# Optimization experiments

Hardware: AMD Instinct MI355X
Metric: run time of the kernel (lower is better)

## Reference

```python
import jax, jax.numpy as jnp
import numpy as np

B, CIN, COUT, L, K = 4, 512, 512, 4096, 7
DIL, STR = 1, 1
OUT_LEN = (L - DIL * (K - 1) - 1) // STR + 1  # 4090 ('valid' conv output length)


def setup_inputs() -> dict:
    key = jax.random.key(0)
    k1, k2, k3, k4 = jax.random.split(key, 4)
    x = jax.random.normal(k1, (B, CIN, L), dtype=jnp.float32)
    offsets = jax.random.normal(k2, (B, 1, OUT_LEN, K), dtype=jnp.float32)
    # kaiming_uniform_(a=sqrt(5)) on [COUT, CIN, K] -> U(-1/sqrt(fan_in), 1/sqrt(fan_in))
    fan_in = CIN * K
    bound = 1.0 / np.sqrt(fan_in)
    weight = jax.random.uniform(k3, (COUT, CIN, K), dtype=jnp.float32, minval=-bound, maxval=bound)
    bias = jax.random.uniform(k4, (COUT,), dtype=jnp.float32, minval=-bound, maxval=bound)
    return {"x": x, "offsets": offsets, "weight": weight, "bias": bias}


def _deform_interp(x, offsets, kernel_size, dilation, stride):
    # x: [B, C, L]; offsets: [B, 1, out_len, K] (offset_groups == 1)
    Lx = x.shape[-1]
    dil_pos = (jnp.arange(kernel_size) * dilation).astype(offsets.dtype)       # [K]
    out_len = offsets.shape[-2]
    t0s = (jnp.arange(out_len) * stride).astype(offsets.dtype)[:, None]        # [out_len, 1]
    T = t0s + dil_pos + offsets                                                # [B, 1, out_len, K]
    # constrained: each sample must stay inside its receptive field
    T = jnp.maximum(T, t0s)
    T = jnp.minimum(T, t0s + dil_pos[-1])
    U0 = jnp.clip(jnp.floor(T).astype(jnp.int32), 0, Lx - 2)                   # [B, 1, out_len, K]
    U = jnp.stack([U0, U0 + 1], axis=-1)                                       # [B, 1, out_len, K, 2]
    idx = U[:, 0]                                                              # [B, out_len, K, 2]
    # gather along length, broadcast index over channels
    xg = jax.vmap(lambda xb, ib: xb[:, ib])(x, idx)                            # [B, C, out_len, K, 2]
    # linear-interp weights: max(0, 1 - |U - T|)
    G = jnp.maximum(0.0, 1.0 - jnp.abs(U.astype(T.dtype) - T[..., None]))      # [B, 1, out_len, K, 2]
    return jnp.sum(G * xg, axis=-1)                                            # [B, C, out_len, K]


def reference(x, offsets, weight, bias):
    samp = _deform_interp(x, offsets, K, DIL, STR)                             # [B, C, out_len, K]
    # conv1d(weight, stride=K) on flattened [B, C, out_len*K] == per-position full contraction
    out = jnp.einsum('bcok,dck->bdo', samp, weight) + bias[:, None]            # [B, COUT, out_len]
    return out
```

## Files before the change

kernel.cpp:

```cpp
#include <hip/hip_runtime.h>
#include <hip/hip_bf16.h>
#include <stdint.h>

#define B_      4
#define CIN     512
#define COUT    512
#define L_      4096
#define K_      7
#define OUT_LEN 4090

typedef unsigned short ushort_t;
typedef __attribute__((ext_vector_type(8))) __bf16 bf16x8;
typedef __attribute__((ext_vector_type(4))) float f32x4;

__device__ __forceinline__ uint32_t f2bf(float f) {
    uint32_t u = __float_as_uint(f);
    return (u + 0x7fffu + ((u >> 16) & 1u)) >> 16;
}

__device__ __forceinline__ uint32_t pack2bf(float s0, float s1) {
    __hip_bfloat162 h = __float22bfloat162_rn(make_float2(s0, s1));
    uint32_t r;
    __builtin_memcpy(&r, &h, 4);
    return r;
}

__device__ __forceinline__ uint32_t interp1(uint32_t wl, uint32_t wh, float g0, float g1) {
    const float l0 = __uint_as_float(wl << 16);
    const float l1 = __uint_as_float(wl & 0xffff0000u);
    const float h0 = __uint_as_float(wh << 16);
    const float h1 = __uint_as_float(wh & 0xffff0000u);
    return pack2bf(g0 * l0 + g1 * h0, g0 * l1 + g1 * h1);
}

__device__ __forceinline__ void async16(const void* g, void* l) {
    __builtin_amdgcn_global_load_lds(
        (const __attribute__((address_space(1))) unsigned int*)g,
        (__attribute__((address_space(3))) unsigned int*)l, 16, 0, 0);
}


__global__ __launch_bounds__(256)
void reorder_w2_kernel(const float* __restrict__ w, uint32_t* __restrict__ Wr) {
    const int d   = blockIdx.x;
    const int tid = threadIdx.x;
    __shared__ float wrow[3584];
    const float4* src = (const float4*)(w + (size_t)d * 3584);
    for (int e = tid; e < 896; e += 256) ((float4*)wrow)[e] = src[e];
    __syncthreads();
    const int cc  = tid >> 4;
    const int clp = tid & 15;
    const int pos = (((clp >> 2) ^ ((d >> 1) & 3)) << 2) | (clp & 3);
    #pragma unroll
    for (int k = 0; k < K_; ++k) {
        const float w0 = wrow[tid * 14 + k];
        const float w1 = wrow[tid * 14 + 7 + k];
        Wr[((size_t)(cc * 7 + k) * 512 + d) * 16 + pos] = (f2bf(w1) << 16) | f2bf(w0);
    }
}

__global__ __launch_bounds__(256)
void interp_pack_kernel(const float* __restrict__ x, const float* __restrict__ offs,
                        uint32_t* __restrict__ P) {
    const int obx = blockIdx.x;
    const int cc  = blockIdx.y;
    const int b   = blockIdx.z;
    const int tid = threadIdx.x;
    const int o0  = obx * 128;
    __shared__ __align__(16) uint32_t XT[2176];

    const float* xc = x + ((size_t)b * CIN + cc * 32) * L_ + o0;
    #pragma unroll
    for (int r = 0; r < 3; ++r) {
        const int e = r * 256 + tid;
        if (e < 544) {
            const int cp   = e / 34;
            const int col4 = e - cp * 34;
            const int colb = col4 * 4;
            const float* p0 = xc + (size_t)(2 * cp) * L_ + colb;
            const float* p1 = p0 + L_;
            float4 v0, v1;
            if (o0 + colb + 3 < L_) {
                v0 = *(const float4*)p0;
                v1 = *(const float4*)p1;
            } else {
                float a0 = (o0 + colb + 0 < L_) ? p0[0] : 0.f;
                float a1 = (o0 + colb + 1 < L_) ? p0[1] : 0.f;
                float a2 = (o0 + colb + 2 < L_) ? p0[2] : 0.f;
                float a3 = (o0 + colb + 3 < L_) ? p0[3] : 0.f;
                float b0 = (o0 + colb + 0 < L_) ? p1[0] : 0.f;
                float b1 = (o0 + colb + 1 < L_) ? p1[1] : 0.f;
                float b2 = (o0 + colb + 2 < L_) ? p1[2] : 0.f;
                float b3 = (o0 + colb + 3 < L_) ? p1[3] : 0.f;
                v0 = make_float4(a0, a1, a2, a3);
                v1 = make_float4(b0, b1, b2, b3);
            }
            const float* f0 = (const float*)&v0;
            const float* f1 = (const float*)&v1;
            const int cpg = cp >> 1, hh = cp & 1;
            #pragma unroll
            for (int ii = 0; ii < 4; ++ii) {
                const int col = colb + ii;
                XT[col * 16 + (((cpg ^ (col & 7)) << 1) | hh)] = pack2bf(f0[ii], f1[ii]);
            }
        }
    }
    __syncthreads();

    const int o_loc = tid >> 1;
    const int h     = tid & 1;
    int o = o0 + o_loc; if (o > OUT_LEN - 1) o = OUT_LEN - 1;
    const float t0f = (float)o;
    const int sr = (o_loc >> 1) & 3;
    uint32_t* Pb = P + ((size_t)((b * 16 + cc) * 7) * 32 + obx) * 2048 + o_loc * 16;
    const int c0 = ((2 * h) ^ sr) << 2;
    const int c1 = ((2 * h + 1) ^ sr) << 2;
    #pragma unroll
    for (int k = 0; k < K_; ++k) {
        const float off = offs[((size_t)b * OUT_LEN + o) * K_ + k];
        float T = t0f + (float)k + off;
        T = fmaxf(T, t0f);
        T = fminf(T, t0f + 6.0f);
        int u0 = (int)floorf(T); if (u0 > L_ - 2) u0 = L_ - 2;
        const float g1 = T - (float)u0;
        const float g0 = 1.0f - g1;
        const int ul = u0 - o0;
        const uint32_t* R0 = &XT[ul * 16];
        const uint32_t* R1 = &XT[(ul + 1) * 16];
        const int s0 = ul & 7, s1 = (ul + 1) & 7;
        uint32_t ow[8];
        #pragma unroll
        for (int q = 0; q < 4; ++q) {
            const int pg = h * 4 + q;
            const uint2 lo = *(const uint2*)&R0[(pg ^ s0) << 1];
            const uint2 hi = *(const uint2*)&R1[(pg ^ s1) << 1];
            ow[q * 2 + 0] = interp1(lo.x, hi.x, g0, g1);
            ow[q * 2 + 1] = interp1(lo.y, hi.y, g0, g1);
        }
        uint32_t* Pk = Pb + (size_t)k * 65536;
        *(uint4*)&Pk[c0] = make_uint4(ow[0], ow[1], ow[2], ow[3]);
        *(uint4*)&Pk[c1] = make_uint4(ow[4], ow[5], ow[6], ow[7]);
    }
}

__global__ __launch_bounds__(512, 1)
void gemm_kernel(const ushort_t* __restrict__ Wr, const uint32_t* __restrict__ P,
                 const float* __restrict__ bias, float* __restrict__ out) {
    const int bxi  = blockIdx.x;
    const int o0   = bxi * 128;
    const int d0   = blockIdx.y * 256;
    const int b    = blockIdx.z;
    const int tid  = threadIdx.x;
    const int wv   = tid >> 6;
    const int lane = tid & 63;
    const int m16  = lane & 15;
    const int quad = lane >> 4;
    const int wd   = wv >> 1;
    const int wo   = wv & 1;
    const int sw   = (m16 >> 1) & 3;
    const int chk  = (quad ^ sw) * 8;

    __shared__ __align__(16) ushort_t As0[8192], As1[8192], As2[8192], As3[8192];
    __shared__ __align__(16) ushort_t Bs0[4096], Bs1[4096], Bs2[4096], Bs3[4096];

    const int aoff = (wd * 64 + m16) * 32 + chk;
    const int boff = (wo * 64 + m16) * 32 + chk;

    const ushort_t* Ag = Wr + (size_t)d0 * 32 + (size_t)tid * 8;
    const uint32_t* Bg = P + ((size_t)(b * 112) * 32 + bxi) * 2048 + (size_t)tid * 4;

#define ISSUE(S, ASP, BSP)                                                    \
    { _Pragma("unroll") for (int r_ = 0; r_ < 2; ++r_)                        \
        async16(Ag + (size_t)(S) * 16384 + r_ * 4096,                         \
                (void*)((ASP) + (r_ * 512 + wv * 64) * 8));                   \
      async16(Bg + (size_t)(S) * 65536,                                       \
              (void*)((BSP) + (size_t)(wv * 64) * 8)); }

#define WAITBAR(N)                                                            \
    { asm volatile("s_waitcnt vmcnt(" #N ")" ::: "memory");                   \
      __builtin_amdgcn_s_barrier();                                           \
      __builtin_amdgcn_sched_barrier(0); }

#define SSTEP(ASP, BSP)                                                       \
    {                                                                         \
        bf16x8 af_[4], bf_[4];                                                \
        _Pragma("unroll")                                                     \
        for (int i_ = 0; i_ < 4; ++i_) af_[i_] = *(const bf16x8*)&(ASP)[aoff + i_ * 512]; \
        _Pragma("unroll")                                                     \
        for (int j_ = 0; j_ < 4; ++j_) bf_[j_] = *(const bf16x8*)&(BSP)[boff + j_ * 512]; \
        __builtin_amdgcn_s_setprio(1);                                        \
        _Pragma("unroll")                                                     \
        for (int i_ = 0; i_ < 4; ++i_) {                                      \
            _Pragma("unroll")                                                 \
            for (int j_ = 0; j_ < 4; ++j_)                                    \
                acc[i_][j_] = __builtin_amdgcn_mfma_f32_16x16x32_bf16(        \
                    af_[i_], bf_[j_], acc[i_][j_], 0, 0, 0);                  \
        }                                                                     \
        __builtin_amdgcn_s_setprio(0);                                        \
    }

    f32x4 acc[4][4];
    #pragma unroll
    for (int i = 0; i < 4; ++i) {
        #pragma unroll
        for (int j = 0; j < 4; ++j) acc[i][j] = (f32x4){0.f, 0.f, 0.f, 0.f};
    }

    ISSUE(0, As0, Bs0);
    ISSUE(1, As1, Bs1);

    #pragma unroll 1
    for (int t = 0; t < 108; t += 4) {
        ISSUE(t + 2, As2, Bs2); WAITBAR(6); SSTEP(As0, Bs0);
        ISSUE(t + 3, As3, Bs3); WAITBAR(6); SSTEP(As1, Bs1);
        ISSUE(t + 4, As0, Bs0); WAITBAR(6); SSTEP(As2, Bs2);
        ISSUE(t + 5, As1, Bs1); WAITBAR(6); SSTEP(As3, Bs3);
    }
    ISSUE(110, As2, Bs2); WAITBAR(6); SSTEP(As0, Bs0);
    ISSUE(111, As3, Bs3); WAITBAR(6); SSTEP(As1, Bs1);
    WAITBAR(3); SSTEP(As2, Bs2);
    WAITBAR(0); SSTEP(As3, Bs3);

    #pragma unroll
    for (int i = 0; i < 4; ++i) {
        const int dd = d0 + wd * 64 + i * 16 + quad * 4;
        float bv[4];
        #pragma unroll
        for (int r = 0; r < 4; ++r) bv[r] = bias[dd + r];
        #pragma unroll
        for (int j = 0; j < 4; ++j) {
            const int oo = o0 + wo * 64 + j * 16 + m16;
            if (oo < OUT_LEN) {
                float* op = out + (size_t)b * COUT * OUT_LEN + (size_t)dd * OUT_LEN + oo;
                #pragma unroll
                for (int r = 0; r < 4; ++r)
                    op[(size_t)r * OUT_LEN] = acc[i][j][r] + bv[r];
            }
        }
    }
#undef ISSUE
#undef WAITBAR
#undef SSTEP
}


__global__ __launch_bounds__(256)
void reorder_w1_kernel(const float* __restrict__ w, uint32_t* __restrict__ Wr) {
    const int d   = blockIdx.x;
    const int tid = threadIdx.x;
    __shared__ float wrow[3584];
    const float4* src = (const float4*)(w + (size_t)d * 3584);
    for (int e = tid; e < 896; e += 256) ((float4*)wrow)[e] = src[e];
    __syncthreads();
    const int cc  = tid >> 4;
    const int clp = tid & 15;
    #pragma unroll
    for (int k = 0; k < K_; ++k) {
        const float w0 = wrow[tid * 14 + k];
        const float w1 = wrow[tid * 14 + 7 + k];
        Wr[((size_t)((k * 16 + cc) * 512 + d)) * 16 + clp] = (f2bf(w1) << 16) | f2bf(w0);
    }
}

__global__ __launch_bounds__(256)
void prepack_kernel(const float* __restrict__ x, uint32_t* __restrict__ xpack) {
    const int obx = blockIdx.x;
    const int cc  = blockIdx.y;
    const int b   = blockIdx.z;
    const int tid = threadIdx.x;
    const int o0  = obx * 128;
    __shared__ __align__(16) uint32_t XT[2176];
    const float* xc = x + ((size_t)b * CIN + cc * 32) * L_ + o0;
    #pragma unroll
    for (int r = 0; r < 3; ++r) {
        const int e = r * 256 + tid;
        if (e < 544) {
            const int cp   = e / 34;
            const int col4 = e - cp * 34;
            const int colb = col4 * 4;
            const float* p0 = xc + (size_t)(2 * cp) * L_ + colb;
            const float* p1 = p0 + L_;
            float4 v0, v1;
            if (o0 + colb + 3 < L_) {
                v0 = *(const float4*)p0;
                v1 = *(const float4*)p1;
            } else {
                float a0 = (o0 + colb + 0 < L_) ? p0[0] : 0.f;
                float a1 = (o0 + colb + 1 < L_) ? p0[1] : 0.f;
                float a2 = (o0 + colb + 2 < L_) ? p0[2] : 0.f;
                float a3 = (o0 + colb + 3 < L_) ? p0[3] : 0.f;
                float b0 = (o0 + colb + 0 < L_) ? p1[0] : 0.f;
                float b1 = (o0 + colb + 1 < L_) ? p1[1] : 0.f;
                float b2 = (o0 + colb + 2 < L_) ? p1[2] : 0.f;
                float b3 = (o0 + colb + 3 < L_) ? p1[3] : 0.f;
                v0 = make_float4(a0, a1, a2, a3);
                v1 = make_float4(b0, b1, b2, b3);
            }
            const float* f0 = (const float*)&v0;
            const float* f1 = (const float*)&v1;
            const int cpg = cp >> 1, h = cp & 1;
            #pragma unroll
            for (int ii = 0; ii < 4; ++ii) {
                const int col = colb + ii;
                XT[col * 16 + (((cpg ^ (col & 7)) << 1) | h)] = pack2bf(f0[ii], f1[ii]);
            }
        }
    }
    __syncthreads();
    uint4* dst = (uint4*)xpack + (size_t)((b * 16 + cc) * 32 + obx) * 544;
    const uint4* s4 = (const uint4*)XT;
    #pragma unroll
    for (int r = 0; r < 3; ++r) {
        const int e = r * 256 + tid;
        if (e < 544) dst[e] = s4[e];
    }
}

__global__ __launch_bounds__(256, 2)
void fused_v1_kernel(const float* __restrict__ offs, const ushort_t* __restrict__ Wr,
                     const uint32_t* __restrict__ xpack, const float* __restrict__ bias,
                     float* __restrict__ out) {
    const int bxi  = blockIdx.x;
    const int o0   = bxi * 128;
    const int d0   = blockIdx.y * 128;
    const int b    = blockIdx.z;
    const int tid  = threadIdx.x;
    const int wv   = tid >> 6;
    const int lane = tid & 63;
    const int m16  = lane & 15;
    const int quad = lane >> 4;
    const int ob   = wv * 32;
    const int q2   = quad * 2;

    __shared__ __align__(16) ushort_t As0[4096], As1[4096], As2[4096], As3[4096];
    __shared__ __align__(16) uint32_t XTB0[2304], XTB1[2304];
    __shared__ int    SU[896];
    __shared__ float2 PG[896];

#define ISSUE_A(KK, CC, ASP)                                                      \
    {                                                                             \
        _Pragma("unroll")                                                         \
        for (int r_ = 0; r_ < 2; ++r_) {                                          \
            const int c_ = r_ * 256 + tid;                                        \
            const int row_ = c_ >> 2, pc_ = c_ & 3;                               \
            const ushort_t* g_ = Wr                                               \
                + ((size_t)(((KK) * 16 + (CC)) * 512 + d0 + row_)) * 32 + pc_ * 8;\
            async16(g_, (void*)((ASP) + (r_ * 256 + wv * 64) * 8));               \
        }                                                                         \
    }

#define ISSUE_XTB(CC, XP)                                                         \
    {                                                                             \
        const uint32_t* sp_ = xpack + ((size_t)((b * 16 + (CC)) * 32 + bxi)) * 2176; \
        _Pragma("unroll")                                                         \
        for (int r_ = 0; r_ < 3; ++r_) {                                          \
            const int cb_ = r_ * 256 + wv * 64;                                   \
            if (cb_ < 544) {                                                      \
                const int c_ = r_ * 256 + tid;                                    \
                async16((const void*)(sp_ + (size_t)c_ * 4),                      \
                        (void*)((XP) + (size_t)cb_ * 4));                         \
            }                                                                     \
        }                                                                         \
    }

#define STEP(KK, XP, ASP)                                                         \
    {                                                                             \
        bf16x8 af_[8];                                                            \
        _Pragma("unroll")                                                         \
        for (int i_ = 0; i_ < 8; ++i_)                                            \
            af_[i_] = *(const bf16x8*)&(ASP)[(i_ * 16 + m16) * 32 + quad * 8];    \
        bf16x8 bfr_[2];                                                           \
        _Pragma("unroll")                                                         \
        for (int j_ = 0; j_ < 2; ++j_) {                                          \
            const int row_ = ((KK) << 7) | (ob + j_ * 16 + m16);                  \
            const int u_ = SU[row_];                                              \
            const float2 g_ = PG[row_];                                           \
            const uint32_t* Xr0_ = &(XP)[u_ * 16];                                \
            const uint32_t* Xr1_ = Xr0_ + 16;                                     \
            const int s0_ = u_ & 7, s1_ = (u_ + 1) & 7;                           \
            const uint2 a0_ = *(const uint2*)&Xr0_[((q2     ^ s0_) << 1)];        \
            const uint2 a1_ = *(const uint2*)&Xr0_[(((q2+1) ^ s0_) << 1)];        \
            const uint2 c0_ = *(const uint2*)&Xr1_[((q2     ^ s1_) << 1)];        \
            const uint2 c1_ = *(const uint2*)&Xr1_[(((q2+1) ^ s1_) << 1)];        \
            uint4 rr_;                                                            \
            rr_.x = interp1(a0_.x, c0_.x, g_.x, g_.y);                            \
            rr_.y = interp1(a0_.y, c0_.y, g_.x, g_.y);                            \
            rr_.z = interp1(a1_.x, c1_.x, g_.x, g_.y);                            \
            rr_.w = interp1(a1_.y, c1_.y, g_.x, g_.y);                            \
            __builtin_memcpy(&bfr_[j_], &rr_, 16);                                \
        }                                                                         \
        _Pragma("unroll")                                                         \
        for (int i_ = 0; i_ < 8; ++i_) {                                          \
            _Pragma("unroll")                                                     \
            for (int j_ = 0; j_ < 2; ++j_)                                        \
                acc[i_][j_] = __builtin_amdgcn_mfma_f32_16x16x32_bf16(af_[i_], bfr_[j_], acc[i_][j_], 0, 0, 0); \
        }                                                                         \
    }

#define HALF(CCB, A0_, A1_, A2_, A3_)                                             \
    ISSUE_A(2, (CCB), A2_); ISSUE_A(3, (CCB), A3_); ISSUE_XTB((CCB) + 1, XTB1);   \
    STEP(0, XTB0, A0_); STEP(1, XTB0, A1_); __syncthreads();                      \
    ISSUE_A(4, (CCB), A0_); ISSUE_A(5, (CCB), A1_);                               \
    STEP(2, XTB0, A2_); STEP(3, XTB0, A3_); __syncthreads();                      \
    ISSUE_A(6, (CCB), A2_); ISSUE_A(0, (CCB) + 1, A3_);                           \
    STEP(4, XTB0, A0_); STEP(5, XTB0, A1_); __syncthreads();                      \
    ISSUE_A(1, (CCB) + 1, A0_); ISSUE_A(2, (CCB) + 1, A1_);                       \
    STEP(6, XTB0, A2_); STEP(0, XTB1, A3_); __syncthreads();                      \
    ISSUE_A(3, (CCB) + 1, A2_); ISSUE_A(4, (CCB) + 1, A3_);                       \
    if ((CCB) + 2 < 16) { ISSUE_XTB((CCB) + 2, XTB0); }                           \
    STEP(1, XTB1, A0_); STEP(2, XTB1, A1_); __syncthreads();                      \
    ISSUE_A(5, (CCB) + 1, A0_); ISSUE_A(6, (CCB) + 1, A1_);                       \
    STEP(3, XTB1, A2_); STEP(4, XTB1, A3_); __syncthreads();                      \
    if ((CCB) + 2 < 16) { ISSUE_A(0, (CCB) + 2, A2_); ISSUE_A(1, (CCB) + 2, A3_); } \
    STEP(5, XTB1, A0_); STEP(6, XTB1, A1_); __syncthreads();

    f32x4 acc[8][2];
    #pragma unroll
    for (int i = 0; i < 8; ++i) {
        #pragma unroll
        for (int j = 0; j < 2; ++j) acc[i][j] = (f32x4){0.f, 0.f, 0.f, 0.f};
    }

    ISSUE_XTB(0, XTB0);
    ISSUE_A(0, 0, As0);
    ISSUE_A(1, 0, As1);
    for (int e = tid; e < 896; e += 256) {
        const int k  = e >> 7;
        const int ol = e & 127;
        int o = o0 + ol; if (o > OUT_LEN - 1) o = OUT_LEN - 1;
        const float t0  = (float)o;
        const float off = offs[((size_t)b * OUT_LEN + o) * K_ + k];
        float T = t0 + (float)k + off;
        T = fmaxf(T, t0);
        T = fminf(T, t0 + 6.0f);
        int u0 = (int)floorf(T);
        if (u0 > L_ - 2) u0 = L_ - 2;
        const float g0 = fmaxf(1.0f - fabsf((float)u0 - T), 0.0f);
        const float g1 = fmaxf(1.0f - fabsf((float)(u0 + 1) - T), 0.0f);
        SU[e] = u0 - o0;
        PG[e] = make_float2(g0, g1);
    }
    __syncthreads();

    #pragma unroll 1
    for (int s4 = 0; s4 < 16; s4 += 4) {
        HALF(s4,     As0, As1, As2, As3)
        HALF(s4 + 2, As2, As3, As0, As1)
    }

    #pragma unroll
    for (int i = 0; i < 8; ++i) {
        const int dd = d0 + i * 16 + quad * 4;
        float bv[4];
        #pragma unroll
        for (int r = 0; r < 4; ++r) bv[r] = bias[dd + r];
        #pragma unroll
        for (int j = 0; j < 2; ++j) {
            const int oo = o0 + ob + j * 16 + m16;
            if (oo < OUT_LEN) {
                float* op = out + (size_t)b * COUT * OUT_LEN + (size_t)dd * OUT_LEN + oo;
                #pragma unroll
                for (int r = 0; r < 4; ++r)
                    op[(size_t)r * OUT_LEN] = acc[i][j][r] + bv[r];
            }
        }
    }
#undef ISSUE_A
#undef ISSUE_XTB
#undef STEP
#undef HALF
}

#define BM 64
#define BN 64
#define BC 8
#define TT (BC * K_)

__global__ __launch_bounds__(256, 2)
void deform_conv1d_fallback(const float* __restrict__ x, const float* __restrict__ offsets,
                            const float* __restrict__ weight, const float* __restrict__ bias,
                            float* __restrict__ out) {
    const int o0 = blockIdx.x * BN, d0 = blockIdx.y * BM, b = blockIdx.z, tid = threadIdx.x;
    __shared__ int   SU[BN * K_];
    __shared__ float SG0[BN * K_], SG1[BN * K_];
    __shared__ float XT[BC][BN + 8];
    __shared__ float S[BC][K_][BN];
    __shared__ float WT[BM][TT + 1];
    for (int e = tid; e < BN * K_; e += 256) {
        const int ol = e / K_, k = e % K_, o = o0 + ol;
        int u0rel = 0; float g0 = 0.f, g1 = 0.f;
        if (o < OUT_LEN) {
            const float t0 = (float)o;
            const float off = offsets[(size_t)b * OUT_LEN * K_ + (size_t)o * K_ + k];
            float T = fminf(fmaxf(t0 + (float)k + off, t0), t0 + 6.0f);
            int u0 = (int)floorf(T); if (u0 > L_ - 2) u0 = L_ - 2;
            g0 = fmaxf(1.0f - fabsf((float)u0 - T), 0.0f);
            g1 = fmaxf(1.0f - fabsf((float)(u0 + 1) - T), 0.0f);
            u0rel = u0 - o0;
        }
        SU[e] = u0rel; SG0[e] = g0; SG1[e] = g1;
    }
    float acc[4][4];
    #pragma unroll
    for (int i = 0; i < 4; ++i) {
        #pragma unroll
        for (int j = 0; j < 4; ++j) acc[i][j] = 0.f;
    }
    const int ty = tid >> 4, tx = tid & 15;
    const float* xb = x + (size_t)b * CIN * L_;
    for (int c0 = 0; c0 < CIN; c0 += BC) {
        __syncthreads();
        for (int e = tid; e < BC * (BN + 7); e += 256) {
            const int cl = e / (BN + 7), j = e % (BN + 7), pos = o0 + j;
            XT[cl][j] = (pos < L_) ? xb[(size_t)(c0 + cl) * L_ + pos] : 0.f;
        }
        for (int e = tid; e < BM * TT; e += 256) {
            const int d = e / TT, t = e % TT;
            WT[d][t] = weight[(size_t)(d0 + d) * (CIN * K_) + c0 * K_ + t];
        }
        __syncthreads();
        for (int e = tid; e < BC * K_ * BN; e += 256) {
            const int cl = e / (K_ * BN), r = e % (K_ * BN), k = r / BN, ol = r % BN;
            const int p = ol * K_ + k, u = SU[p];
            S[cl][k][ol] = SG0[p] * XT[cl][u] + SG1[p] * XT[cl][u + 1];
        }
        __syncthreads();
        #pragma unroll
        for (int t = 0; t < TT; ++t) {
            const int cl = t / K_, k = t % K_;
            const float4 s4 = *(const float4*)&S[cl][k][tx * 4];
            const float w0 = WT[ty * 4 + 0][t], w1 = WT[ty * 4 + 1][t];
            const float w2 = WT[ty * 4 + 2][t], w3 = WT[ty * 4 + 3][t];
            acc[0][0] += w0 * s4.x; acc[0][1] += w0 * s4.y; acc[0][2] += w0 * s4.z; acc[0][3] += w0 * s4.w;
            acc[1][0] += w1 * s4.x; acc[1][1] += w1 * s4.y; acc[1][2] += w1 * s4.z; acc[1][3] += w1 * s4.w;
            acc[2][0] += w2 * s4.x; acc[2][1] += w2 * s4.y; acc[2][2] += w2 * s4.z; acc[2][3] += w2 * s4.w;
            acc[3][0] += w3 * s4.x; acc[3][1] += w3 * s4.y; acc[3][2] += w3 * s4.z; acc[3][3] += w3 * s4.w;
        }
    }
    #pragma unroll
    for (int i = 0; i < 4; ++i) {
        const int d = d0 + ty * 4 + i;
        const float bvv = bias[d];
        #pragma unroll
        for (int j = 0; j < 4; ++j) {
            const int o = o0 + tx * 4 + j;
            if (o < OUT_LEN)
                out[(size_t)b * COUT * OUT_LEN + (size_t)d * OUT_LEN + o] = acc[i][j] + bvv;
        }
    }
}

extern "C" void kernel_launch(void* const* d_in, const int* in_sizes, int n_in,
                              void* d_out, int out_size, void* d_ws, size_t ws_size,
                              hipStream_t stream) {
    const float* x       = (const float*)d_in[0];
    const float* offsets = (const float*)d_in[1];
    const float* weight  = (const float*)d_in[2];
    const float* bias    = (const float*)d_in[3];
    float* out = (float*)d_out;

    const size_t WR_BYTES = (size_t)512 * 512 * 7 * 2;
    const size_t P_BYTES  = (size_t)4 * 16 * 7 * 32 * 8192;
    const size_t XP_BYTES = (size_t)2048 * 544 * 16 + 512;

    if (ws_size >= WR_BYTES + P_BYTES) {
        uint32_t* Wr_u32 = (uint32_t*)d_ws;
        ushort_t* Wr     = (ushort_t*)d_ws;
        uint32_t* P      = (uint32_t*)((char*)d_ws + WR_BYTES);
        reorder_w2_kernel<<<512, 256, 0, stream>>>(weight, Wr_u32);
        interp_pack_kernel<<<dim3(32, 16, B_), 256, 0, stream>>>(x, offsets, P);
        gemm_kernel<<<dim3(32, 2, B_), 512, 0, stream>>>(Wr, P, bias, out);
        return;
    }

    if (ws_size >= WR_BYTES + XP_BYTES) {
        uint32_t* Wr_u32 = (uint32_t*)d_ws;
        ushort_t* Wr     = (ushort_t*)d_ws;
        uint32_t* xpack  = (uint32_t*)((char*)d_ws + WR_BYTES);
        reorder_w1_kernel<<<512, 256, 0, stream>>>(weight, Wr_u32);
        prepack_kernel<<<dim3(32, 16, B_), 256, 0, stream>>>(x, xpack);
        fused_v1_kernel<<<dim3(32, 4, B_), 256, 0, stream>>>(offsets, Wr, xpack, bias, out);
        return;
    }

    dim3 grid((OUT_LEN + BN - 1) / BN, COUT / BM, B_);
    deform_conv1d_fallback<<<grid, 256, 0, stream>>>(x, offsets, weight, bias, out);
}
```

Measured before the change: 172.5 us.

## Split MFMA step into two half-slabs with interleaved LDS loads and prefetch

Restructures the GEMM main loop so each K-step is split into two halves. Each half loads part of the B fragments from LDS, issues the next global->LDS prefetch between the LDS reads and the barrier, and runs 8 MFMAs. The prefetch depth grows to three stages in flight, so LDS reads overlap with MFMA execution and global loads. The cost is extra barriers per step and tighter hand-written waitcnt and buffer-reuse logic that could race if a count is wrong.

```diff
diff --git a/kernel.cpp b/kernel.cpp
--- a/kernel.cpp
+++ b/kernel.cpp
@@ -176,27 +176,44 @@
       async16(Bg + (size_t)(S) * 65536,                                       \
               (void*)((BSP) + (size_t)(wv * 64) * 8)); }
 
-#define WAITBAR(N)                                                            \
-    { asm volatile("s_waitcnt vmcnt(" #N ")" ::: "memory");                   \
-      __builtin_amdgcn_s_barrier();                                           \
-      __builtin_amdgcn_sched_barrier(0); }
-
-#define SSTEP(ASP, BSP)                                                       \
+#define SLAB(ASP, BSP, DOI, SN, ANX, BNX, VN)                                 \
     {                                                                         \
-        bf16x8 af_[4], bf_[4];                                                \
+        bf16x8 af_[4], bA_[2], bB_[2];                                        \
+         \
         _Pragma("unroll")                                                     \
         for (int i_ = 0; i_ < 4; ++i_) af_[i_] = *(const bf16x8*)&(ASP)[aoff + i_ * 512]; \
-        _Pragma("unroll")                                                     \
-        for (int j_ = 0; j_ < 4; ++j_) bf_[j_] = *(const bf16x8*)&(BSP)[boff + j_ * 512]; \
+        bA_[0] = *(const bf16x8*)&(BSP)[boff];                                \
+        bA_[1] = *(const bf16x8*)&(BSP)[boff + 512];                          \
+        __builtin_amdgcn_sched_barrier(0);                                    \
+        if (DOI) { ISSUE(SN, ANX, BNX); }                                     \
+        __builtin_amdgcn_s_barrier();                                         \
+        asm volatile("s_waitcnt lgkmcnt(0)" ::: "memory");                    \
+        __builtin_amdgcn_sched_barrier(0);                                    \
         __builtin_amdgcn_s_setprio(1);                                        \
         _Pragma("unroll")                                                     \
         for (int i_ = 0; i_ < 4; ++i_) {                                      \
-            _Pragma("unroll")                                                 \
-            for (int j_ = 0; j_ < 4; ++j_)                                    \
-                acc[i_][j_] = __builtin_amdgcn_mfma_f32_16x16x32_bf16(        \
-                    af_[i_], bf_[j_], acc[i_][j_], 0, 0, 0);                  \
+            acc[i_][0] = __builtin_amdgcn_mfma_f32_16x16x32_bf16(af_[i_], bA_[0], acc[i_][0], 0, 0, 0); \
+            acc[i_][1] = __builtin_amdgcn_mfma_f32_16x16x32_bf16(af_[i_], bA_[1], acc[i_][1], 0, 0, 0); \
         }                                                                     \
         __builtin_amdgcn_s_setprio(0);                                        \
+                     \
+        bB_[0] = *(const bf16x8*)&(BSP)[boff + 1024];                         \
+        bB_[1] = *(const bf16x8*)&(BSP)[boff + 1536];                         \
+        __builtin_amdgcn_sched_barrier(0);                                    \
+        __builtin_amdgcn_s_barrier();                                         \
+        asm volatile("s_waitcnt lgkmcnt(0)" ::: "memory");                    \
+        __builtin_amdgcn_sched_barrier(0);                                    \
+        __builtin_amdgcn_s_setprio(1);                                        \
+        _Pragma("unroll")                                                     \
+        for (int i_ = 0; i_ < 4; ++i_) {                                      \
+            acc[i_][2] = __builtin_amdgcn_mfma_f32_16x16x32_bf16(af_[i_], bB_[0], acc[i_][2], 0, 0, 0); \
+            acc[i_][3] = __builtin_amdgcn_mfma_f32_16x16x32_bf16(af_[i_], bB_[1], acc[i_][3], 0, 0, 0); \
+        }                                                                     \
+        __builtin_amdgcn_s_setprio(0);                                        \
+         \
+        asm volatile("s_waitcnt vmcnt(" VN ")" ::: "memory");                 \
+        __builtin_amdgcn_s_barrier();                                         \
+        __builtin_amdgcn_sched_barrier(0);                                    \
     }
 
     f32x4 acc[4][4];
@@ -208,18 +225,22 @@
 
     ISSUE(0, As0, Bs0);
     ISSUE(1, As1, Bs1);
+    ISSUE(2, As2, Bs2);
+    asm volatile("s_waitcnt vmcnt(6)" ::: "memory");
+    __builtin_amdgcn_s_barrier();
+    __builtin_amdgcn_sched_barrier(0);
 
     #pragma unroll 1
     for (int t = 0; t < 108; t += 4) {
-        ISSUE(t + 2, As2, Bs2); WAITBAR(6); SSTEP(As0, Bs0);
-        ISSUE(t + 3, As3, Bs3); WAITBAR(6); SSTEP(As1, Bs1);
-        ISSUE(t + 4, As0, Bs0); WAITBAR(6); SSTEP(As2, Bs2);
-        ISSUE(t + 5, As1, Bs1); WAITBAR(6); SSTEP(As3, Bs3);
-    }
-    ISSUE(110, As2, Bs2); WAITBAR(6); SSTEP(As0, Bs0);
-    ISSUE(111, As3, Bs3); WAITBAR(6); SSTEP(As1, Bs1);
-    WAITBAR(3); SSTEP(As2, Bs2);
-    WAITBAR(0); SSTEP(As3, Bs3);
+        SLAB(As0, Bs0, 1, t + 3, As3, Bs3, "6")
+        SLAB(As1, Bs1, 1, t + 4, As0, Bs0, "6")
+        SLAB(As2, Bs2, 1, t + 5, As1, Bs1, "6")
+        SLAB(As3, Bs3, 1, t + 6, As2, Bs2, "6")
+    }
+    SLAB(As0, Bs0, 1, 111, As3, Bs3, "6")
+    SLAB(As1, Bs1, 0, 0, As0, Bs0, "3")
+    SLAB(As2, Bs2, 0, 0, As0, Bs0, "0")
+    SLAB(As3, Bs3, 0, 0, As0, Bs0, "0")
 
     #pragma unroll
     for (int i = 0; i < 4; ++i) {
@@ -239,8 +260,7 @@
         }
     }
 #undef ISSUE
-#undef WAITBAR
-#undef SSTEP
+#undef SLAB
 }
 
 
```

Result: no change. 169.8 us, median of 2 (-1.6%).
